# Performance work log

Measured on AMD Instinct MI355X. Metric: run time of the kernel, lower is better.

Reference implementation:

```python
import jax, jax.numpy as jnp
import numpy as np

N = 50000      # nodes
E = 800000     # edges (avg degree 16)
D_IN = 128     # node_feature_dim
H = 256        # hidden_dim
EPS = 1e-5     # BatchNorm eps


def setup_inputs() -> dict:
    key = jax.random.key(0)
    ks = jax.random.split(key, 32)
    inp = {
        "x": jax.random.normal(ks[0], (N, D_IN), jnp.float32),
        "edge_index": jax.random.randint(ks[1], (2, E), 0, N, jnp.int32),
    }
    dims = [(D_IN, H), (H, H), (H, H)]
    k = 2
    for i, (din, dout) in enumerate(dims):
        s = 1.0 / np.sqrt(din)
        inp[f"Wl{i}"] = jax.random.uniform(ks[k], (din, dout), jnp.float32, -s, s); k += 1
        inp[f"bl{i}"] = jax.random.uniform(ks[k], (dout,), jnp.float32, -s, s); k += 1
        inp[f"Wr{i}"] = jax.random.uniform(ks[k], (din, dout), jnp.float32, -s, s); k += 1
        inp[f"g{i}"] = jnp.ones((dout,), jnp.float32)
        inp[f"b{i}"] = jnp.zeros((dout,), jnp.float32)
        inp[f"rm{i}"] = jax.random.normal(ks[k], (dout,), jnp.float32) * 0.1; k += 1
        inp[f"rv{i}"] = jax.random.uniform(ks[k], (dout,), jnp.float32, 0.5, 1.5); k += 1
    return inp


def _sage(x, src, dst, Wl, bl, Wr):
    # PyG SAGEConv (aggr='mean'): out = lin_l(mean_{j in N(i)} x_j) + lin_r(x_i)
    deg = jax.ops.segment_sum(jnp.ones((src.shape[0],), x.dtype), dst, num_segments=N)
    agg = jax.ops.segment_sum(x[src], dst, num_segments=N)  # [N, d_in]
    mean = agg / jnp.maximum(deg, 1.0)[:, None]
    return mean @ Wl + bl + x @ Wr


def _bn(x, g, b, rm, rv):
    # eval-mode BatchNorm1d with running stats
    return (x - rm) * (g * jax.lax.rsqrt(rv + EPS)) + b


def reference(x, edge_index,
              Wl0, bl0, Wr0, g0, b0, rm0, rv0,
              Wl1, bl1, Wr1, g1, b1, rm1, rv1,
              Wl2, bl2, Wr2, g2, b2, rm2, rv2):
    src, dst = edge_index[0], edge_index[1]
    h = jax.nn.relu(_bn(_sage(x, src, dst, Wl0, bl0, Wr0), g0, b0, rm0, rv0))
    h = jax.nn.relu(_bn(_sage(h, src, dst, Wl1, bl1, Wr1), g1, b1, rm1, rv1))
    h = _bn(_sage(h, src, dst, Wl2, bl2, Wr2), g2, b2, rm2, rv2)
    return h  # [N, H] node embeddings (dropout is identity in eval mode)
```

## Files before the change

### kernel.cpp

```cpp
#include <hip/hip_runtime.h>
#include <hip/hip_bf16.h>

#define NNODES 50000
#define NEDGES 800000
#define HID 256
#define BN_EPS 1e-5f
#define SCAN_B ((NNODES + 255) / 256)

typedef __attribute__((ext_vector_type(8))) short short8v;
typedef __attribute__((ext_vector_type(4))) float f32x4;

__device__ inline void load_lds16(const void* g, void* l) {
    __builtin_amdgcn_global_load_lds(
        (const __attribute__((address_space(1))) unsigned int*)g,
        (__attribute__((address_space(3))) unsigned int*)l, 16, 0, 0);
}

__global__ void k_zero(int* p, int n) {
    int i = blockIdx.x * blockDim.x + threadIdx.x;
    if (i < n) p[i] = 0;
}

__global__ void k_countrank(const int* __restrict__ ei, int* __restrict__ cnt,
                            int* __restrict__ rank, int nE) {
    int e = blockIdx.x * blockDim.x + threadIdx.x;
    if (e < nE) rank[e] = atomicAdd(&cnt[ei[nE + e]], 1);
}

__global__ void k_bsum(const int* __restrict__ cnt, int* __restrict__ loc,
                       int* __restrict__ bsum, int n) {
    __shared__ int sh[256];
    int tid = threadIdx.x;
    int i = blockIdx.x * 256 + tid;
    int v = (i < n) ? cnt[i] : 0;
    sh[tid] = v;
    __syncthreads();
    for (int off = 1; off < 256; off <<= 1) {
        int t = (tid >= off) ? sh[tid - off] : 0;
        __syncthreads();
        sh[tid] += t;
        __syncthreads();
    }
    if (i < n) loc[i] = sh[tid] - v;
    if (tid == 255) bsum[blockIdx.x] = sh[255];
}

__global__ void k_bscan(int* __restrict__ bsum, int nb) {
    __shared__ int sh[256];
    int tid = threadIdx.x;
    int v = (tid < nb) ? bsum[tid] : 0;
    sh[tid] = v;
    __syncthreads();
    for (int off = 1; off < 256; off <<= 1) {
        int t = (tid >= off) ? sh[tid - off] : 0;
        __syncthreads();
        sh[tid] += t;
        __syncthreads();
    }
    if (tid < nb) bsum[tid] = sh[tid] - v;
}

__global__ void k_addoff(const int* __restrict__ loc, const int* __restrict__ bsum,
                         int* __restrict__ rowptr, int n, int nE) {
    int i = blockIdx.x * 256 + threadIdx.x;
    if (i < n) rowptr[i] = loc[i] + bsum[blockIdx.x];
    if (i == 0) rowptr[n] = nE;
}

__global__ void k_fill2(const int* __restrict__ ei, const int* __restrict__ rowptr,
                        const int* __restrict__ rank, int* __restrict__ col, int nE) {
    int e = blockIdx.x * blockDim.x + threadIdx.x;
    if (e < nE) col[rowptr[ei[nE + e]] + rank[e]] = ei[e];
}

__global__ void k_cast(const float* __restrict__ in, __hip_bfloat16* __restrict__ out, int n) {
    int i = blockIdx.x * blockDim.x + threadIdx.x;
    int base = i * 4;
    if (base + 3 < n) {
        float4 v = *(const float4*)(in + base);
        out[base + 0] = __float2bfloat16(v.x);
        out[base + 1] = __float2bfloat16(v.y);
        out[base + 2] = __float2bfloat16(v.z);
        out[base + 3] = __float2bfloat16(v.w);
    } else {
        for (int j = base; j < n; j++) out[j] = __float2bfloat16(in[j]);
    }
}

__global__ void k_transpose6(const float* __restrict__ s0, const float* __restrict__ s1,
                             const float* __restrict__ s2, const float* __restrict__ s3,
                             const float* __restrict__ s4, const float* __restrict__ s5,
                             __hip_bfloat16* __restrict__ d0, __hip_bfloat16* __restrict__ d1,
                             __hip_bfloat16* __restrict__ d2, __hip_bfloat16* __restrict__ d3,
                             __hip_bfloat16* __restrict__ d4, __hip_bfloat16* __restrict__ d5) {
    int f = blockIdx.x * blockDim.x + threadIdx.x;
    const float* src; __hip_bfloat16* dst; int K; int i;
    if (f < 65536) {
        K = 128;
        if (f < 32768) { src = s0; dst = d0; i = f; }
        else           { src = s1; dst = d1; i = f - 32768; }
    } else {
        K = 256;
        int r = f - 65536;
        int wsel = r >> 16;
        i = r & 65535;
        src = (wsel == 0) ? s2 : (wsel == 1) ? s3 : (wsel == 2) ? s4 : s5;
        dst = (wsel == 0) ? d2 : (wsel == 1) ? d3 : (wsel == 2) ? d4 : d5;
    }
    int k = i >> 8;
    int nn = i & 255;
    dst[nn * K + k] = __float2bfloat16(src[i]);
}

template <int D, int U>
__global__ void k_meanh(const __hip_bfloat16* __restrict__ xin,
                        const int* __restrict__ rowptr, const int* __restrict__ col,
                        __hip_bfloat16* __restrict__ mean, int n, int fo) {
    constexpr int QPR = D / 8;
    int gw = (blockIdx.x * blockDim.x + threadIdx.x) >> 6;
    int lane = threadIdx.x & 63;
    if (gw >= n) return;
    int beg = rowptr[gw], end = rowptr[gw + 1];
    int sub = lane >> 4;
    int fpos = lane & 15;
    const uint4* base = (const uint4*)xin;
    int foq = fo >> 3;

    float acc[8];
#pragma unroll
    for (int j = 0; j < 8; j++) acc[j] = 0.f;

    for (int p0 = beg; p0 < end; p0 += U * 4) {
        int idx[U]; bool ok[U];
#pragma unroll
        for (int u = 0; u < U; u++) {
            int p = p0 + u * 4 + sub;
            ok[u] = (p < end);
            idx[u] = ok[u] ? col[p] : 0;
        }
        uint4 v[U];
#pragma unroll
        for (int u = 0; u < U; u++) {
            uint4 t = {0u, 0u, 0u, 0u};
            if (ok[u]) t = base[(size_t)idx[u] * QPR + foq + fpos];
            v[u] = t;
        }
#pragma unroll
        for (int u = 0; u < U; u++) {
            const unsigned int uu[4] = {v[u].x, v[u].y, v[u].z, v[u].w};
#pragma unroll
            for (int j = 0; j < 4; j++) {
                acc[2 * j]     += __uint_as_float(uu[j] << 16);
                acc[2 * j + 1] += __uint_as_float(uu[j] & 0xffff0000u);
            }
        }
    }

#pragma unroll
    for (int j = 0; j < 8; j++) acc[j] += __shfl_xor(acc[j], 32, 64);
#pragma unroll
    for (int j = 0; j < 8; j++) acc[j] += __shfl_xor(acc[j], 16, 64);

    if (sub == 0) {
        float inv = (end > beg) ? 1.f / (float)(end - beg) : 0.f;
        union { uint4 v; unsigned short s[8]; } o;
#pragma unroll
        for (int j = 0; j < 8; j++)
            o.s[j] = __bfloat16_as_ushort(__float2bfloat16(acc[j] * inv));
        *(uint4*)(mean + (size_t)gw * D + fo + fpos * 8) = o.v;
    }
}

template <int K, typename OutT, int RELU>
__launch_bounds__(256, 2)
__global__ void k_gemm2(const __hip_bfloat16* __restrict__ A1,
                        const __hip_bfloat16* __restrict__ A2,
                        const __hip_bfloat16* __restrict__ W1t,
                        const __hip_bfloat16* __restrict__ W2t,
                        const float* __restrict__ bl,
                        const float* __restrict__ g,
                        const float* __restrict__ bb,
                        const float* __restrict__ rm,
                        const float* __restrict__ rv,
                        OutT* __restrict__ out, int n) {
    __shared__ __hip_bfloat16 As1[128 * 32];
    __shared__ __hip_bfloat16 As2[128 * 32];
    __shared__ __hip_bfloat16 Bs1[256 * 32];
    __shared__ __hip_bfloat16 Bs2[256 * 32];
    int tid = threadIdx.x;
    int lane = tid & 63;
    int w = tid >> 6;
    int quad = lane >> 4;
    int ml = lane & 15;
    int rowBase = blockIdx.x * 128;
    int wr = w >> 1, wc = w & 1;

    f32x4 acc[4][8];
#pragma unroll
    for (int i = 0; i < 4; i++)
#pragma unroll
        for (int t = 0; t < 8; t++) acc[i][t] = {0.f, 0.f, 0.f, 0.f};

    int srow = tid >> 2;
    int sbyte = (tid & 3) * 16;

    for (int k0 = 0; k0 < K; k0 += 32) {
        __syncthreads();
#pragma unroll
        for (int h = 0; h < 2; h++) {
            int r = srow + h * 64;
            int grow = rowBase + r; if (grow >= n) grow = n - 1;
            load_lds16((const char*)(A1 + (size_t)grow * K + k0) + sbyte,
                       (char*)As1 + r * 64 + sbyte);
            load_lds16((const char*)(A2 + (size_t)grow * K + k0) + sbyte,
                       (char*)As2 + r * 64 + sbyte);
        }
#pragma unroll
        for (int h = 0; h < 4; h++) {
            int c = srow + h * 64;
            load_lds16((const char*)(W1t + (size_t)c * K + k0) + sbyte,
                       (char*)Bs1 + c * 64 + sbyte);
            load_lds16((const char*)(W2t + (size_t)c * K + k0) + sbyte,
                       (char*)Bs2 + c * 64 + sbyte);
        }
        __syncthreads();

        short8v af1[4], af2[4];
#pragma unroll
        for (int i = 0; i < 4; i++) {
            af1[i] = *(const short8v*)(As1 + (wr * 64 + i * 16 + ml) * 32 + quad * 8);
            af2[i] = *(const short8v*)(As2 + (wr * 64 + i * 16 + ml) * 32 + quad * 8);
        }
#pragma unroll
        for (int t = 0; t < 8; t++) {
            short8v bf1 = *(const short8v*)(Bs1 + (wc * 128 + t * 16 + ml) * 32 + quad * 8);
            short8v bf2 = *(const short8v*)(Bs2 + (wc * 128 + t * 16 + ml) * 32 + quad * 8);
#pragma unroll
            for (int i = 0; i < 4; i++) {
                acc[i][t] = __builtin_amdgcn_mfma_f32_16x16x32_bf16(af1[i], bf1, acc[i][t], 0, 0, 0);
                acc[i][t] = __builtin_amdgcn_mfma_f32_16x16x32_bf16(af2[i], bf2, acc[i][t], 0, 0, 0);
            }
        }
    }

#pragma unroll
    for (int t = 0; t < 8; t++) {
        int c = wc * 128 + t * 16 + ml;
        float sv = g[c] * rsqrtf(rv[c] + BN_EPS);
        float tv = (bl[c] - rm[c]) * sv + bb[c];
#pragma unroll
        for (int i = 0; i < 4; i++) {
            int row0 = rowBase + wr * 64 + i * 16 + quad * 4;
#pragma unroll
            for (int r = 0; r < 4; r++) {
                int row = row0 + r;
                if (row < n) {
                    float v = acc[i][t][r] * sv + tv;
                    if (RELU) v = fmaxf(v, 0.f);
                    if constexpr (sizeof(OutT) == 2)
                        out[(size_t)row * HID + c] = (OutT)__float2bfloat16(v);
                    else
                        out[(size_t)row * HID + c] = (OutT)v;
                }
            }
        }
    }
}

extern "C" void kernel_launch(void* const* d_in, const int* in_sizes, int n_in,
                              void* d_out, int out_size, void* d_ws, size_t ws_size,
                              hipStream_t stream) {
    const float* x = (const float*)d_in[0];
    const int* ei = (const int*)d_in[1];
    const float *Wl[3], *blv[3], *Wr[3], *g[3], *bb[3], *rm[3], *rv[3];
    for (int i = 0; i < 3; i++) {
        int b = 2 + i * 7;
        Wl[i]  = (const float*)d_in[b + 0];
        blv[i] = (const float*)d_in[b + 1];
        Wr[i]  = (const float*)d_in[b + 2];
        g[i]   = (const float*)d_in[b + 3];
        bb[i]  = (const float*)d_in[b + 4];
        rm[i]  = (const float*)d_in[b + 5];
        rv[i]  = (const float*)d_in[b + 6];
    }

    char* ob = (char*)d_out;
    __hip_bfloat16* xb = (__hip_bfloat16*)ob;
    __hip_bfloat16* h0 = (__hip_bfloat16*)(ob + (size_t)NNODES * 128 * 2);

    char* w = (char*)d_ws;
    size_t off = 0;
    auto alloc = [&](size_t bytes) {
        void* p = w + off;
        off += (bytes + 255) & ~(size_t)255;
        return p;
    };
    int* rowptr = (int*)alloc((NNODES + 1) * sizeof(int));
    int* cnt    = (int*)alloc(NNODES * sizeof(int));
    int* loc    = (int*)alloc(NNODES * sizeof(int));
    int* bsum   = (int*)alloc(SCAN_B * sizeof(int));
    int* rank   = (int*)alloc(NEDGES * sizeof(int));
    int* col    = (int*)alloc(NEDGES * sizeof(int));
    __hip_bfloat16* meanb = (__hip_bfloat16*)alloc((size_t)NNODES * HID * 2);
    __hip_bfloat16* h1    = (__hip_bfloat16*)alloc((size_t)NNODES * HID * 2);
    __hip_bfloat16* Wt[6];
    int Ks[6] = {128, 128, 256, 256, 256, 256};
    for (int i = 0; i < 6; i++) Wt[i] = (__hip_bfloat16*)alloc((size_t)Ks[i] * HID * 2);

    k_zero<<<SCAN_B, 256, 0, stream>>>(cnt, NNODES);
    k_countrank<<<(NEDGES + 255) / 256, 256, 0, stream>>>(ei, cnt, rank, NEDGES);
    k_bsum<<<SCAN_B, 256, 0, stream>>>(cnt, loc, bsum, NNODES);
    k_bscan<<<1, 256, 0, stream>>>(bsum, SCAN_B);
    k_addoff<<<SCAN_B, 256, 0, stream>>>(loc, bsum, rowptr, NNODES, NEDGES);
    k_fill2<<<(NEDGES + 255) / 256, 256, 0, stream>>>(ei, rowptr, rank, col, NEDGES);

    k_cast<<<(NNODES * 128 / 4 + 255) / 256, 256, 0, stream>>>(x, xb, NNODES * 128);

    k_transpose6<<<(327680 + 255) / 256, 256, 0, stream>>>(
        Wl[0], Wr[0], Wl[1], Wr[1], Wl[2], Wr[2],
        Wt[0], Wt[1], Wt[2], Wt[3], Wt[4], Wt[5]);

    int meanBlocks = (NNODES * 64 + 255) / 256;
    int gemmBlocks = (NNODES + 127) / 128;

    k_meanh<128, 4><<<meanBlocks, 256, 0, stream>>>(xb, rowptr, col, meanb, NNODES, 0);
    k_gemm2<128, __hip_bfloat16, 1><<<gemmBlocks, 256, 0, stream>>>(meanb, xb, Wt[0], Wt[1],
        blv[0], g[0], bb[0], rm[0], rv[0], h0, NNODES);

    k_meanh<256, 4><<<meanBlocks, 256, 0, stream>>>(h0, rowptr, col, meanb, NNODES, 0);
    k_meanh<256, 4><<<meanBlocks, 256, 0, stream>>>(h0, rowptr, col, meanb, NNODES, 128);
    k_gemm2<256, __hip_bfloat16, 1><<<gemmBlocks, 256, 0, stream>>>(meanb, h0, Wt[2], Wt[3],
        blv[1], g[1], bb[1], rm[1], rv[1], h1, NNODES);

    k_meanh<256, 4><<<meanBlocks, 256, 0, stream>>>(h1, rowptr, col, meanb, NNODES, 0);
    k_meanh<256, 4><<<meanBlocks, 256, 0, stream>>>(h1, rowptr, col, meanb, NNODES, 128);
    k_gemm2<256, float, 0><<<gemmBlocks, 256, 0, stream>>>(meanb, h1, Wt[4], Wt[5],
        blv[2], g[2], bb[2], rm[2], rv[2], (float*)d_out, NNODES);
}
```

Measured before the change: 411.2 us.

## Gather neighbor features in FP8 and fuse prep kernels into one launch

Adds FP8 copies of the input features and of each hidden layer. The first two GEMM epilogues write them alongside the bf16 outputs, and the mean-aggregation kernels gather these FP8 rows instead of bf16. This halves the bytes of the random-access gather and lets one pass cover all 256 features instead of two passes of 128. The cast, weight transpose and count zeroing are merged into a single prep kernel. The costs are lower precision in the aggregated means and extra byte-wise scattered stores in the GEMM epilogue.

```diff
diff --git a/kernel.cpp b/kernel.cpp
--- a/kernel.cpp
+++ b/kernel.cpp
@@ -9,16 +9,12 @@
 
 typedef __attribute__((ext_vector_type(8))) short short8v;
 typedef __attribute__((ext_vector_type(4))) float f32x4;
+typedef __attribute__((ext_vector_type(2))) float f32x2;
 
 __device__ inline void load_lds16(const void* g, void* l) {
     __builtin_amdgcn_global_load_lds(
         (const __attribute__((address_space(1))) unsigned int*)g,
         (__attribute__((address_space(3))) unsigned int*)l, 16, 0, 0);
-}
-
-__global__ void k_zero(int* p, int n) {
-    int i = blockIdx.x * blockDim.x + threadIdx.x;
-    if (i < n) p[i] = 0;
 }
 
 __global__ void k_countrank(const int* __restrict__ ei, int* __restrict__ cnt,
@@ -73,68 +69,76 @@
     if (e < nE) col[rowptr[ei[nE + e]] + rank[e]] = ei[e];
 }
 
-__global__ void k_cast(const float* __restrict__ in, __hip_bfloat16* __restrict__ out, int n) {
-    int i = blockIdx.x * blockDim.x + threadIdx.x;
-    int base = i * 4;
-    if (base + 3 < n) {
-        float4 v = *(const float4*)(in + base);
-        out[base + 0] = __float2bfloat16(v.x);
-        out[base + 1] = __float2bfloat16(v.y);
-        out[base + 2] = __float2bfloat16(v.z);
-        out[base + 3] = __float2bfloat16(v.w);
+#define PREP_CAST 1600000
+#define PREP_TR   327680
+__global__ void k_prep(const float* __restrict__ x,
+                       __hip_bfloat16* __restrict__ xb, unsigned char* __restrict__ x8,
+                       const float* __restrict__ s0, const float* __restrict__ s1,
+                       const float* __restrict__ s2, const float* __restrict__ s3,
+                       const float* __restrict__ s4, const float* __restrict__ s5,
+                       __hip_bfloat16* __restrict__ d0, __hip_bfloat16* __restrict__ d1,
+                       __hip_bfloat16* __restrict__ d2, __hip_bfloat16* __restrict__ d3,
+                       __hip_bfloat16* __restrict__ d4, __hip_bfloat16* __restrict__ d5,
+                       int* __restrict__ cnt) {
+    int f = blockIdx.x * blockDim.x + threadIdx.x;
+    if (f < PREP_CAST) {
+        float4 v = *(const float4*)(x + f * 4);
+        union { uint2 u; unsigned short s[4]; } ob;
+        ob.s[0] = __bfloat16_as_ushort(__float2bfloat16(v.x));
+        ob.s[1] = __bfloat16_as_ushort(__float2bfloat16(v.y));
+        ob.s[2] = __bfloat16_as_ushort(__float2bfloat16(v.z));
+        ob.s[3] = __bfloat16_as_ushort(__float2bfloat16(v.w));
+        *(uint2*)(xb + f * 4) = ob.u;
+        int p = __builtin_amdgcn_cvt_pk_fp8_f32(v.x, v.y, 0, false);
+        p = __builtin_amdgcn_cvt_pk_fp8_f32(v.z, v.w, p, true);
+        *(int*)(x8 + f * 4) = p;
+    } else if (f < PREP_CAST + PREP_TR) {
+        int r = f - PREP_CAST;
+        const float* src; __hip_bfloat16* dst; int K; int i;
+        if (r < 65536) {
+            K = 128;
+            if (r < 32768) { src = s0; dst = d0; i = r; }
+            else           { src = s1; dst = d1; i = r - 32768; }
+        } else {
+            K = 256;
+            int q = r - 65536;
+            int wsel = q >> 16;
+            i = q & 65535;
+            src = (wsel == 0) ? s2 : (wsel == 1) ? s3 : (wsel == 2) ? s4 : s5;
+            dst = (wsel == 0) ? d2 : (wsel == 1) ? d3 : (wsel == 2) ? d4 : d5;
+        }
+        int k = i >> 8;
+        int nn = i & 255;
+        dst[nn * K + k] = __float2bfloat16(src[i]);
     } else {
-        for (int j = base; j < n; j++) out[j] = __float2bfloat16(in[j]);
-    }
-}
-
-__global__ void k_transpose6(const float* __restrict__ s0, const float* __restrict__ s1,
-                             const float* __restrict__ s2, const float* __restrict__ s3,
-                             const float* __restrict__ s4, const float* __restrict__ s5,
-                             __hip_bfloat16* __restrict__ d0, __hip_bfloat16* __restrict__ d1,
-                             __hip_bfloat16* __restrict__ d2, __hip_bfloat16* __restrict__ d3,
-                             __hip_bfloat16* __restrict__ d4, __hip_bfloat16* __restrict__ d5) {
-    int f = blockIdx.x * blockDim.x + threadIdx.x;
-    const float* src; __hip_bfloat16* dst; int K; int i;
-    if (f < 65536) {
-        K = 128;
-        if (f < 32768) { src = s0; dst = d0; i = f; }
-        else           { src = s1; dst = d1; i = f - 32768; }
-    } else {
-        K = 256;
-        int r = f - 65536;
-        int wsel = r >> 16;
-        i = r & 65535;
-        src = (wsel == 0) ? s2 : (wsel == 1) ? s3 : (wsel == 2) ? s4 : s5;
-        dst = (wsel == 0) ? d2 : (wsel == 1) ? d3 : (wsel == 2) ? d4 : d5;
-    }
-    int k = i >> 8;
-    int nn = i & 255;
-    dst[nn * K + k] = __float2bfloat16(src[i]);
+        int i = f - PREP_CAST - PREP_TR;
+        if (i < NNODES) cnt[i] = 0;
+    }
 }
 
 template <int D, int U>
-__global__ void k_meanh(const __hip_bfloat16* __restrict__ xin,
-                        const int* __restrict__ rowptr, const int* __restrict__ col,
-                        __hip_bfloat16* __restrict__ mean, int n, int fo) {
-    constexpr int QPR = D / 8;
+__global__ void k_meanf8(const unsigned char* __restrict__ x8,
+                         const int* __restrict__ rowptr, const int* __restrict__ col,
+                         __hip_bfloat16* __restrict__ mean, int n) {
+    constexpr int CPL = D / 16;
+    constexpr int R = 64 / CPL;
     int gw = (blockIdx.x * blockDim.x + threadIdx.x) >> 6;
     int lane = threadIdx.x & 63;
     if (gw >= n) return;
     int beg = rowptr[gw], end = rowptr[gw + 1];
-    int sub = lane >> 4;
-    int fpos = lane & 15;
-    const uint4* base = (const uint4*)xin;
-    int foq = fo >> 3;
-
-    float acc[8];
-#pragma unroll
-    for (int j = 0; j < 8; j++) acc[j] = 0.f;
-
-    for (int p0 = beg; p0 < end; p0 += U * 4) {
+    int sub = lane / CPL;
+    int fpos = lane % CPL;
+    const uint4* base = (const uint4*)x8;
+
+    float acc[16];
+#pragma unroll
+    for (int j = 0; j < 16; j++) acc[j] = 0.f;
+
+    for (int p0 = beg; p0 < end; p0 += U * R) {
         int idx[U]; bool ok[U];
 #pragma unroll
         for (int u = 0; u < U; u++) {
-            int p = p0 + u * 4 + sub;
+            int p = p0 + u * R + sub;
             ok[u] = (p < end);
             idx[u] = ok[u] ? col[p] : 0;
         }
@@ -142,36 +146,46 @@
 #pragma unroll
         for (int u = 0; u < U; u++) {
             uint4 t = {0u, 0u, 0u, 0u};
-            if (ok[u]) t = base[(size_t)idx[u] * QPR + foq + fpos];
+            if (ok[u]) t = base[(size_t)idx[u] * CPL + fpos];
             v[u] = t;
         }
 #pragma unroll
         for (int u = 0; u < U; u++) {
             const unsigned int uu[4] = {v[u].x, v[u].y, v[u].z, v[u].w};
 #pragma unroll
-            for (int j = 0; j < 4; j++) {
-                acc[2 * j]     += __uint_as_float(uu[j] << 16);
-                acc[2 * j + 1] += __uint_as_float(uu[j] & 0xffff0000u);
+            for (int q = 0; q < 4; q++) {
+                f32x2 lo = __builtin_amdgcn_cvt_pk_f32_fp8(uu[q], false);
+                f32x2 hi = __builtin_amdgcn_cvt_pk_f32_fp8(uu[q], true);
+                acc[4 * q + 0] += lo.x;
+                acc[4 * q + 1] += lo.y;
+                acc[4 * q + 2] += hi.x;
+                acc[4 * q + 3] += hi.y;
             }
         }
     }
 
-#pragma unroll
-    for (int j = 0; j < 8; j++) acc[j] += __shfl_xor(acc[j], 32, 64);
-#pragma unroll
-    for (int j = 0; j < 8; j++) acc[j] += __shfl_xor(acc[j], 16, 64);
+    if constexpr (R >= 8) {
+#pragma unroll
+        for (int j = 0; j < 16; j++) acc[j] += __shfl_xor(acc[j], 8, 64);
+    }
+#pragma unroll
+    for (int j = 0; j < 16; j++) acc[j] += __shfl_xor(acc[j], 16, 64);
+#pragma unroll
+    for (int j = 0; j < 16; j++) acc[j] += __shfl_xor(acc[j], 32, 64);
 
     if (sub == 0) {
         float inv = (end > beg) ? 1.f / (float)(end - beg) : 0.f;
-        union { uint4 v; unsigned short s[8]; } o;
-#pragma unroll
-        for (int j = 0; j < 8; j++)
+        union { uint4 v[2]; unsigned short s[16]; } o;
+#pragma unroll
+        for (int j = 0; j < 16; j++)
             o.s[j] = __bfloat16_as_ushort(__float2bfloat16(acc[j] * inv));
-        *(uint4*)(mean + (size_t)gw * D + fo + fpos * 8) = o.v;
-    }
-}
-
-template <int K, typename OutT, int RELU>
+        uint4* dst = (uint4*)(mean + (size_t)gw * D + fpos * 16);
+        dst[0] = o.v[0];
+        dst[1] = o.v[1];
+    }
+}
+
+template <int K, typename OutT, int RELU, int W8>
 __launch_bounds__(256, 2)
 __global__ void k_gemm2(const __hip_bfloat16* __restrict__ A1,
                         const __hip_bfloat16* __restrict__ A2,
@@ -182,7 +196,8 @@
                         const float* __restrict__ bb,
                         const float* __restrict__ rm,
                         const float* __restrict__ rv,
-                        OutT* __restrict__ out, int n) {
+                        OutT* __restrict__ out, unsigned char* __restrict__ out8,
+                        int n) {
     __shared__ __hip_bfloat16 As1[128 * 32];
     __shared__ __hip_bfloat16 As2[128 * 32];
     __shared__ __hip_bfloat16 Bs1[256 * 32];
@@ -261,6 +276,10 @@
                         out[(size_t)row * HID + c] = (OutT)__float2bfloat16(v);
                     else
                         out[(size_t)row * HID + c] = (OutT)v;
+                    if constexpr (W8) {
+                        int p = __builtin_amdgcn_cvt_pk_fp8_f32(v, v, 0, false);
+                        out8[(size_t)row * HID + c] = (unsigned char)(p & 0xFF);
+                    }
                 }
             }
         }
@@ -303,37 +322,36 @@
     int* col    = (int*)alloc(NEDGES * sizeof(int));
     __hip_bfloat16* meanb = (__hip_bfloat16*)alloc((size_t)NNODES * HID * 2);
     __hip_bfloat16* h1    = (__hip_bfloat16*)alloc((size_t)NNODES * HID * 2);
+    unsigned char* x8   = (unsigned char*)alloc((size_t)NNODES * 128);
+    unsigned char* h0f8 = (unsigned char*)alloc((size_t)NNODES * HID);
+    unsigned char* h1f8 = (unsigned char*)alloc((size_t)NNODES * HID);
     __hip_bfloat16* Wt[6];
     int Ks[6] = {128, 128, 256, 256, 256, 256};
     for (int i = 0; i < 6; i++) Wt[i] = (__hip_bfloat16*)alloc((size_t)Ks[i] * HID * 2);
 
-    k_zero<<<SCAN_B, 256, 0, stream>>>(cnt, NNODES);
+    int prepTotal = PREP_CAST + PREP_TR + NNODES;
+    k_prep<<<(prepTotal + 255) / 256, 256, 0, stream>>>(
+        x, xb, x8, Wl[0], Wr[0], Wl[1], Wr[1], Wl[2], Wr[2],
+        Wt[0], Wt[1], Wt[2], Wt[3], Wt[4], Wt[5], cnt);
+
     k_countrank<<<(NEDGES + 255) / 256, 256, 0, stream>>>(ei, cnt, rank, NEDGES);
     k_bsum<<<SCAN_B, 256, 0, stream>>>(cnt, loc, bsum, NNODES);
     k_bscan<<<1, 256, 0, stream>>>(bsum, SCAN_B);
     k_addoff<<<SCAN_B, 256, 0, stream>>>(loc, bsum, rowptr, NNODES, NEDGES);
     k_fill2<<<(NEDGES + 255) / 256, 256, 0, stream>>>(ei, rowptr, rank, col, NEDGES);
 
-    k_cast<<<(NNODES * 128 / 4 + 255) / 256, 256, 0, stream>>>(x, xb, NNODES * 128);
-
-    k_transpose6<<<(327680 + 255) / 256, 256, 0, stream>>>(
-        Wl[0], Wr[0], Wl[1], Wr[1], Wl[2], Wr[2],
-        Wt[0], Wt[1], Wt[2], Wt[3], Wt[4], Wt[5]);
-
     int meanBlocks = (NNODES * 64 + 255) / 256;
     int gemmBlocks = (NNODES + 127) / 128;
 
-    k_meanh<128, 4><<<meanBlocks, 256, 0, stream>>>(xb, rowptr, col, meanb, NNODES, 0);
-    k_gemm2<128, __hip_bfloat16, 1><<<gemmBlocks, 256, 0, stream>>>(meanb, xb, Wt[0], Wt[1],
-        blv[0], g[0], bb[0], rm[0], rv[0], h0, NNODES);
-
-    k_meanh<256, 4><<<meanBlocks, 256, 0, stream>>>(h0, rowptr, col, meanb, NNODES, 0);
-    k_meanh<256, 4><<<meanBlocks, 256, 0, stream>>>(h0, rowptr, col, meanb, NNODES, 128);
-    k_gemm2<256, __hip_bfloat16, 1><<<gemmBlocks, 256, 0, stream>>>(meanb, h0, Wt[2], Wt[3],
-        blv[1], g[1], bb[1], rm[1], rv[1], h1, NNODES);
-
-    k_meanh<256, 4><<<meanBlocks, 256, 0, stream>>>(h1, rowptr, col, meanb, NNODES, 0);
-    k_meanh<256, 4><<<meanBlocks, 256, 0, stream>>>(h1, rowptr, col, meanb, NNODES, 128);
-    k_gemm2<256, float, 0><<<gemmBlocks, 256, 0, stream>>>(meanb, h1, Wt[4], Wt[5],
-        blv[2], g[2], bb[2], rm[2], rv[2], (float*)d_out, NNODES);
-}
+    k_meanf8<128, 2><<<meanBlocks, 256, 0, stream>>>(x8, rowptr, col, meanb, NNODES);
+    k_gemm2<128, __hip_bfloat16, 1, 1><<<gemmBlocks, 256, 0, stream>>>(meanb, xb, Wt[0], Wt[1],
+        blv[0], g[0], bb[0], rm[0], rv[0], h0, h0f8, NNODES);
+
+    k_meanf8<256, 4><<<meanBlocks, 256, 0, stream>>>(h0f8, rowptr, col, meanb, NNODES);
+    k_gemm2<256, __hip_bfloat16, 1, 1><<<gemmBlocks, 256, 0, stream>>>(meanb, h0, Wt[2], Wt[3],
+        blv[1], g[1], bb[1], rm[1], rv[1], h1, h1f8, NNODES);
+
+    k_meanf8<256, 4><<<meanBlocks, 256, 0, stream>>>(h1f8, rowptr, col, meanb, NNODES);
+    k_gemm2<256, float, 0, 0><<<gemmBlocks, 256, 0, stream>>>(meanb, h1, Wt[4], Wt[5],
+        blv[2], g[2], bb[2], rm[2], rv[2], (float*)d_out, (unsigned char*)nullptr, NNODES);
+}
```

New measurement: 376.0 us. -8.6%, faster.
